# Kernel tuning notes

Measured on AMD Instinct MI355X. Metric: run time of the kernel, lower is better.

## Reference

```python
import jax, jax.numpy as jnp
import numpy as np

HIDDEN = 1024
ATT = 512

def _xavier(key, shape):
    fan_in, fan_out = shape[0], shape[1]
    bound = float(np.sqrt(6.0 / (fan_in + fan_out)))
    return jax.random.uniform(key, shape, jnp.float32, -bound, bound)

def setup_inputs() -> dict:
    key = jax.random.key(0)
    ks = jax.random.split(key, 7)
    B, P = 256, 196
    spatial_image = jax.random.normal(ks[0], (B, P, HIDDEN), jnp.float32)
    decoder_out = jax.random.normal(ks[1], (B, HIDDEN), jnp.float32)
    st = jax.random.normal(ks[2], (B, HIDDEN), jnp.float32)
    # weights stored as (in_dim, out_dim); math identical to torch Linear(x @ W.T)
    W_cnn = _xavier(ks[3], (HIDDEN, ATT))
    W_dec = _xavier(ks[4], (HIDDEN, ATT))
    W_sen = _xavier(ks[5], (HIDDEN, ATT))
    W_att = _xavier(ks[6], (ATT, 1))
    return {"spatial_image": spatial_image, "decoder_out": decoder_out, "st": st,
            "W_cnn": W_cnn, "W_dec": W_dec, "W_sen": W_sen, "W_att": W_att}

def reference(spatial_image, decoder_out, st, W_cnn, W_dec, W_sen, W_att):
    # dropout in eval mode (identity)
    cnn_out = jnp.einsum('bph,ha->bpa', spatial_image, W_cnn)   # (B,P,A)
    dec_out = decoder_out @ W_dec                                # (B,A)
    addition = jnp.tanh(cnn_out + dec_out[:, None, :])           # (B,P,A)
    zt = jnp.einsum('bpa,a->bp', addition, W_att[:, 0])          # (B,P)
    alpha_t = jax.nn.softmax(zt, axis=1)                         # (B,P)
    ct = jnp.einsum('bph,bp->bh', spatial_image, alpha_t)        # (B,H)
    sen = jnp.tanh(dec_out + st @ W_sen)                         # (B,A)
    out = sen @ W_att                                            # (B,1)
    concat = jnp.concatenate([zt, out], axis=1)                  # (B,P+1)
    alpha_hat = jax.nn.softmax(concat, axis=1)
    beta_t = alpha_hat[:, -1:]                                   # (B,1)
    c_hat = beta_t * st + (1.0 - beta_t) * ct                    # (B,H)
    return (alpha_t, beta_t, c_hat)
```

## Files before the change

kernel.cpp:

```cpp
#include <hip/hip_runtime.h>
#include <hip/hip_bf16.h>

#define BATCH   256
#define NP      196
#define HIDDEN  1024
#define ATT     512
#define M_TOTAL (BATCH * NP)
#define BM 128
#define BN 128
#define BK 32
#define NB_TILES (ATT / BN)
#define MT_TILES (M_TOTAL / BM)

typedef __attribute__((ext_vector_type(8))) short bf16x8v;
typedef __attribute__((ext_vector_type(4))) float f32x4;

__device__ inline unsigned short f2bf(float x) {
    unsigned int u = __float_as_uint(x);
    u += 0x7fffu + ((u >> 16) & 1u);
    return (unsigned short)(u >> 16);
}

__device__ __forceinline__ unsigned int pk2bf(float lo, float hi) {
    unsigned int r;
    asm("v_cvt_pk_bf16_f32 %0, %1, %2" : "=v"(r) : "v"(lo), "v"(hi));
    return r;
}

__device__ inline float fast_tanh(float x) {
    float e = __expf(2.0f * x);
    return 1.0f - 2.0f / (e + 1.0f);
}

__device__ __forceinline__ void glds16(const void* gsrc, void* ldst) {
    __builtin_amdgcn_global_load_lds(
        (const __attribute__((address_space(1))) unsigned int*)gsrc,
        (__attribute__((address_space(3))) unsigned int*)ldst,
        16, 0, 0);
}

__global__ void k0_arrange(const float* __restrict__ Wc, unsigned short* __restrict__ Wt) {
    int g = blockIdx.x * 256 + threadIdx.x;
    int nb   = g >> 14;
    int kt   = (g >> 9) & 31;
    int col  = (g >> 2) & 127;
    int slot = g & 3;
    int c    = slot ^ ((col & 7) >> 1);
    int kb   = kt * 32 + c * 8;
    int colg = nb * 128 + col;
    unsigned short v[8];
#pragma unroll
    for (int j = 0; j < 8; ++j) v[j] = f2bf(Wc[(size_t)(kb + j) * ATT + colg]);
    uint4 pk;
    pk.x = (unsigned int)v[0] | ((unsigned int)v[1] << 16);
    pk.y = (unsigned int)v[2] | ((unsigned int)v[3] << 16);
    pk.z = (unsigned int)v[4] | ((unsigned int)v[5] << 16);
    pk.w = (unsigned int)v[6] | ((unsigned int)v[7] << 16);
    *(uint4*)(Wt + (size_t)g * 8) = pk;
}

__global__ void k1_small(const float* __restrict__ dec_in, const float* __restrict__ st,
                         const float* __restrict__ Wdec,  const float* __restrict__ Wsen,
                         float* __restrict__ dec_out, float* __restrict__ stw) {
    const float* X = blockIdx.z ? st   : dec_in;
    const float* W = blockIdx.z ? Wsen : Wdec;
    float*       O = blockIdx.z ? stw  : dec_out;
    int ci = threadIdx.x & 31;
    int c0 = blockIdx.x * 128 + ci * 4;
    int b  = blockIdx.y * 8 + (threadIdx.x >> 5);
    const float* x = X + (size_t)b * HIDDEN;
    float4 acc = {0.f, 0.f, 0.f, 0.f};
    for (int k = 0; k < HIDDEN; k += 4) {
#pragma unroll
        for (int kk = 0; kk < 4; ++kk) {
            float4 w = *(const float4*)(W + (size_t)(k + kk) * ATT + c0);
            float a = x[k + kk];
            acc.x += a * w.x; acc.y += a * w.y; acc.z += a * w.z; acc.w += a * w.w;
        }
    }
    *(float4*)(O + (size_t)b * ATT + c0) = acc;
}

__global__ void __launch_bounds__(256, 3)
k2_fused_gemm(const float* __restrict__ A, const unsigned short* __restrict__ Wt,
              const float* __restrict__ dec, const float* __restrict__ Watt,
              float* __restrict__ ztp) {
    __shared__ __align__(16) char Abuf[2][8192];
    __shared__ __align__(16) char Bbuf[2][8192];
    __shared__ float zred[256];

    const int tid = threadIdx.x;
    const int w  = tid >> 6;
    const int l  = tid & 63;
    const int lg = l >> 4, ll = l & 15;
    const int wr = w >> 1, wc = w & 1;

    const int bid = (int)blockIdx.x;
    const int swz = (bid & 7) * 196 + (bid >> 3);
    const int mt = swz >> 2, nb = swz & 3;
    const int r0 = mt * BM;
    const int c0 = nb * BN;

    f32x4 acc[4][4];
#pragma unroll
    for (int m = 0; m < 4; ++m)
#pragma unroll
        for (int n = 0; n < 4; ++n) acc[m][n] = (f32x4){0.f, 0.f, 0.f, 0.f};

    const float* asrc = A + (size_t)(r0 + (tid >> 3)) * HIDDEN + (tid & 7) * 4;
    const int aw_off = ((tid >> 3) * 64)
                     + (((((tid >> 1) & 3) ^ ((tid >> 4) & 3))) << 4)
                     + ((tid & 1) * 8);

    const char* bimg = (const char*)Wt + (size_t)nb * (32 * 8192) + tid * 16;

    float4 avA[4], avB[4];

#define ALOADN(t, av) do {                                                     \
    _Pragma("unroll")                                                          \
    for (int j = 0; j < 4; ++j)                                                \
        (av)[j] = *(const float4*)(asrc + (size_t)j * 32 * HIDDEN + (t) * 32); \
} while (0)

#define BGLDS(t, buf) do {                                                     \
    glds16(bimg + (size_t)(t) * 8192,        (buf) + tid * 16);                \
    glds16(bimg + (size_t)(t) * 8192 + 4096, (buf) + 4096 + tid * 16);         \
} while (0)

#define AWRITE(av, buf) do {                                                   \
    _Pragma("unroll")                                                          \
    for (int j = 0; j < 4; ++j) {                                              \
        uint2 u;                                                               \
        u.x = pk2bf((av)[j].x, (av)[j].y);                                     \
        u.y = pk2bf((av)[j].z, (av)[j].w);                                     \
        *(uint2*)((buf) + j * 2048 + aw_off) = u;                              \
    }                                                                          \
} while (0)

#define COMPUTE(Ab, Bb) do {                                                   \
    const int fx = (ll >> 1) & 3;                                              \
    bf16x8v af[4], bfr[4];                                                     \
    _Pragma("unroll")                                                          \
    for (int m = 0; m < 4; ++m)                                                \
        af[m] = *(const bf16x8v*)((Ab) + (wr * 64 + m * 16 + ll) * 64 +        \
                                  ((lg ^ fx) << 4));                           \
    _Pragma("unroll")                                                          \
    for (int n = 0; n < 4; ++n)                                                \
        bfr[n] = *(const bf16x8v*)((Bb) + (wc * 64 + n * 16 + ll) * 64 +       \
                                   ((lg ^ fx) << 4));                          \
    _Pragma("unroll")                                                          \
    for (int m = 0; m < 4; ++m)                                                \
        _Pragma("unroll")                                                      \
        for (int n = 0; n < 4; ++n)                                            \
            acc[m][n] = __builtin_amdgcn_mfma_f32_16x16x32_bf16(               \
                af[m], bfr[n], acc[m][n], 0, 0, 0);                            \
} while (0)

#define WAITC asm volatile("s_waitcnt vmcnt(4) lgkmcnt(0)" ::: "memory")
#define BAR   __builtin_amdgcn_s_barrier()

    BGLDS(0, Bbuf[0]);
    ALOADN(0, avA);
    ALOADN(1, avB);
    AWRITE(avA, Abuf[0]);
    WAITC;
    BAR;

    for (int tp = 0; tp < 15; ++tp) {
        const int t = tp * 2;
        BGLDS(t + 1, Bbuf[1]);
        ALOADN(t + 2, avA);
        COMPUTE(Abuf[0], Bbuf[0]);
        AWRITE(avB, Abuf[1]);
        WAITC; BAR;
        BGLDS(t + 2, Bbuf[0]);
        ALOADN((t + 3 > 31 ? 31 : t + 3), avB);
        COMPUTE(Abuf[1], Bbuf[1]);
        AWRITE(avA, Abuf[0]);
        WAITC; BAR;
    }
    BGLDS(31, Bbuf[1]);
    COMPUTE(Abuf[0], Bbuf[0]);
    AWRITE(avB, Abuf[1]);
    asm volatile("s_waitcnt vmcnt(0) lgkmcnt(0)" ::: "memory");
    BAR;
    COMPUTE(Abuf[1], Bbuf[1]);

#undef ALOADN
#undef BGLDS
#undef AWRITE
#undef COMPUTE
#undef WAITC
#undef BAR

    const int clocal = wc * 64 + ll;
    float watt[4];
#pragma unroll
    for (int n = 0; n < 4; ++n) watt[n] = Watt[c0 + clocal + n * 16];

#pragma unroll
    for (int m = 0; m < 4; ++m) {
#pragma unroll
        for (int j = 0; j < 4; ++j) {
            int rl = wr * 64 + m * 16 + lg * 4 + j;
            int rowg = r0 + rl;
            int b = rowg / NP;
            const float* db = dec + (size_t)b * ATT + c0;
            float s = 0.f;
#pragma unroll
            for (int n = 0; n < 4; ++n)
                s += fast_tanh(acc[m][n][j] + db[clocal + n * 16]) * watt[n];
            s += __shfl_xor(s, 1);
            s += __shfl_xor(s, 2);
            s += __shfl_xor(s, 4);
            s += __shfl_xor(s, 8);
            if (ll == 0) zred[rl * 2 + wc] = s;
        }
    }
    __syncthreads();
    if (tid < 128) {
        float t = zred[tid * 2] + zred[tid * 2 + 1];
        ztp[(size_t)nb * M_TOTAL + r0 + tid] = t;
    }
}

__global__ void k3_softmax(const float* __restrict__ dec, const float* __restrict__ stw,
                           const float* __restrict__ Watt, const float* __restrict__ ztp,
                           float* __restrict__ out, float* __restrict__ beta_ws) {
    int b = blockIdx.x;
    int t = threadIdx.x;
    __shared__ float red[256];

    float p = 0.f;
#pragma unroll
    for (int c = t; c < ATT; c += 256)
        p += fast_tanh(dec[(size_t)b * ATT + c] + stw[(size_t)b * ATT + c]) * Watt[c];
    red[t] = p;
    __syncthreads();
    for (int s = 128; s > 0; s >>= 1) { if (t < s) red[t] += red[t + s]; __syncthreads(); }
    float outv = red[0];
    __syncthreads();

    float z = -1e30f;
    if (t < NP) {
        z = ztp[b * NP + t] + ztp[M_TOTAL + b * NP + t]
          + ztp[2 * M_TOTAL + b * NP + t] + ztp[3 * M_TOTAL + b * NP + t];
    }
    red[t] = z;
    __syncthreads();
    for (int s = 128; s > 0; s >>= 1) { if (t < s) red[t] = fmaxf(red[t], red[t + s]); __syncthreads(); }
    float m1 = red[0];
    __syncthreads();

    float e = (t < NP) ? __expf(z - m1) : 0.f;
    red[t] = e;
    __syncthreads();
    for (int s = 128; s > 0; s >>= 1) { if (t < s) red[t] += red[t + s]; __syncthreads(); }
    float s1 = red[0];

    if (t < NP) out[b * NP + t] = e / s1;

    if (t == 0) {
        float m2 = fmaxf(m1, outv);
        float s2 = s1 * __expf(m1 - m2) + __expf(outv - m2);
        float beta = __expf(outv - m2) / s2;
        out[M_TOTAL + b] = beta;
        beta_ws[b] = beta;
    }
}

__global__ void k4_ct(const float* __restrict__ spatial, const float* __restrict__ alpha,
                      float* __restrict__ ctp) {
    int q = blockIdx.x;
    int b = blockIdx.y;
    int t = threadIdx.x;
    __shared__ float al[49];
    if (t < 49) al[t] = alpha[b * NP + q * 49 + t];
    __syncthreads();
    const float* sp = spatial + (size_t)b * NP * HIDDEN + (size_t)q * 49 * HIDDEN + t * 4;
    float4 acc = {0.f, 0.f, 0.f, 0.f};
#pragma unroll 7
    for (int p = 0; p < 49; ++p) {
        float4 v = *(const float4*)(sp + (size_t)p * HIDDEN);
        float a = al[p];
        acc.x += a * v.x; acc.y += a * v.y; acc.z += a * v.z; acc.w += a * v.w;
    }
    *(float4*)(ctp + ((size_t)q * BATCH + b) * HIDDEN + t * 4) = acc;
}

__global__ void k5_chat(const float* __restrict__ st, const float* __restrict__ ctp,
                        const float* __restrict__ beta, float* __restrict__ chat) {
    int g = blockIdx.x * 256 + threadIdx.x;
    int b = g >> 8;
    int h0 = (g & 255) * 4;
    float be = beta[b];
    float4 s = *(const float4*)(st + (size_t)b * HIDDEN + h0);
    float4 c = {0.f, 0.f, 0.f, 0.f};
#pragma unroll
    for (int q = 0; q < 4; ++q) {
        float4 v = *(const float4*)(ctp + ((size_t)q * BATCH + b) * HIDDEN + h0);
        c.x += v.x; c.y += v.y; c.z += v.z; c.w += v.w;
    }
    float4 o;
    o.x = be * s.x + (1.f - be) * c.x;
    o.y = be * s.y + (1.f - be) * c.y;
    o.z = be * s.z + (1.f - be) * c.z;
    o.w = be * s.w + (1.f - be) * c.w;
    *(float4*)(chat + (size_t)b * HIDDEN + h0) = o;
}

extern "C" void kernel_launch(void* const* d_in, const int* in_sizes, int n_in,
                              void* d_out, int out_size, void* d_ws, size_t ws_size,
                              hipStream_t stream) {
    const float* spatial = (const float*)d_in[0];
    const float* decoder = (const float*)d_in[1];
    const float* st      = (const float*)d_in[2];
    const float* Wcnn    = (const float*)d_in[3];
    const float* Wdec    = (const float*)d_in[4];
    const float* Wsen    = (const float*)d_in[5];
    const float* Watt    = (const float*)d_in[6];
    float* out = (float*)d_out;

    char* ws = (char*)d_ws;
    unsigned short* Wt = (unsigned short*)(ws + 0);
    float* ztp  = (float*)(ws + 1048576);
    float* dec  = (float*)(ws + 1851392);
    float* stw  = (float*)(ws + 2375680);
    float* beta = (float*)(ws + 2899968);
    float* ctp  = (float*)(ws + 2901504);

    k0_arrange<<<256, 256, 0, stream>>>(Wcnn, Wt);
    k1_small<<<dim3(4, 32, 2), 256, 0, stream>>>(decoder, st, Wdec, Wsen, dec, stw);
    k2_fused_gemm<<<MT_TILES * NB_TILES, 256, 0, stream>>>(spatial, Wt, dec, Watt, ztp);
    k3_softmax<<<256, 256, 0, stream>>>(dec, stw, Watt, ztp, out, beta);
    k4_ct<<<dim3(4, 256), 256, 0, stream>>>(spatial, out, ctp);
    k5_chat<<<256, 256, 0, stream>>>(st, ctp, beta, out + M_TOTAL + BATCH);
}
```

Measured before the change: 199.0 us.

## Pre-convert spatial activations to swizzled bf16 tiles before the GEMM

Adds a pre-pass kernel that converts the fp32 spatial input into bf16 tiles in the same swizzled layout the GEMM uses in LDS. The GEMM then loads both operands straight into LDS with direct global-to-LDS copies, replacing the in-register conversion path. The new GEMM uses a single LDS buffer with two barriers per k-step instead of double buffering. This costs an extra full read and write pass over the activations and loses load/compute overlap, in exchange for halving A bytes inside the GEMM. The new path runs only when the workspace is large enough; otherwise the old kernel is used.

```diff
diff --git a/kernel.cpp b/kernel.cpp
--- a/kernel.cpp
+++ b/kernel.cpp
@@ -8,7 +8,6 @@
 #define M_TOTAL (BATCH * NP)
 #define BM 128
 #define BN 128
-#define BK 32
 #define NB_TILES (ATT / BN)
 #define MT_TILES (M_TOTAL / BM)
 
@@ -57,6 +56,26 @@
     pk.z = (unsigned int)v[4] | ((unsigned int)v[5] << 16);
     pk.w = (unsigned int)v[6] | ((unsigned int)v[7] << 16);
     *(uint4*)(Wt + (size_t)g * 8) = pk;
+}
+
+__global__ void k_pre(const float* __restrict__ sp, unsigned short* __restrict__ Ab) {
+    int g = blockIdx.x * 256 + threadIdx.x;
+    int mt   = g >> 14;
+    int r14  = g & 16383;
+    int kt   = r14 >> 9;
+    int r9   = r14 & 511;
+    int row  = r9 >> 2;
+    int slog = r9 & 3;
+    const float* src = sp + (size_t)(mt * 128 + row) * HIDDEN + kt * 32 + slog * 8;
+    float4 a = *(const float4*)(src);
+    float4 b = *(const float4*)(src + 4);
+    uint4 u;
+    u.x = pk2bf(a.x, a.y);
+    u.y = pk2bf(a.z, a.w);
+    u.z = pk2bf(b.x, b.y);
+    u.w = pk2bf(b.z, b.w);
+    int sphys = slog ^ ((row & 7) >> 1);
+    *(uint4*)((char*)Ab + (size_t)mt * 262144 + kt * 8192 + row * 64 + sphys * 16) = u;
 }
 
 __global__ void k1_small(const float* __restrict__ dec_in, const float* __restrict__ st,
@@ -82,11 +101,11 @@
 }
 
 __global__ void __launch_bounds__(256, 3)
-k2_fused_gemm(const float* __restrict__ A, const unsigned short* __restrict__ Wt,
-              const float* __restrict__ dec, const float* __restrict__ Watt,
-              float* __restrict__ ztp) {
-    __shared__ __align__(16) char Abuf[2][8192];
-    __shared__ __align__(16) char Bbuf[2][8192];
+k2_gemm(const unsigned short* __restrict__ Ab, const unsigned short* __restrict__ Wt,
+        const float* __restrict__ dec, const float* __restrict__ Watt,
+        float* __restrict__ ztp) {
+    __shared__ __align__(16) char As[8192];
+    __shared__ __align__(16) char Bs[8192];
     __shared__ float zred[256];
 
     const int tid = threadIdx.x;
@@ -107,11 +126,93 @@
 #pragma unroll
         for (int n = 0; n < 4; ++n) acc[m][n] = (f32x4){0.f, 0.f, 0.f, 0.f};
 
+    const char* aimg = (const char*)Ab + (size_t)mt * 262144;
+    const char* bimg = (const char*)Wt + (size_t)nb * 262144;
+    const int fx = (ll >> 1) & 3;
+
+    for (int kt = 0; kt < 32; ++kt) {
+        __syncthreads();
+        glds16(aimg + kt * 8192 +        tid * 16, As +        tid * 16);
+        glds16(aimg + kt * 8192 + 4096 + tid * 16, As + 4096 + tid * 16);
+        glds16(bimg + kt * 8192 +        tid * 16, Bs +        tid * 16);
+        glds16(bimg + kt * 8192 + 4096 + tid * 16, Bs + 4096 + tid * 16);
+        __syncthreads();
+
+        bf16x8v af[4], bfr[4];
+#pragma unroll
+        for (int m = 0; m < 4; ++m)
+            af[m] = *(const bf16x8v*)(As + (wr * 64 + m * 16 + ll) * 64 + ((lg ^ fx) << 4));
+#pragma unroll
+        for (int n = 0; n < 4; ++n)
+            bfr[n] = *(const bf16x8v*)(Bs + (wc * 64 + n * 16 + ll) * 64 + ((lg ^ fx) << 4));
+#pragma unroll
+        for (int m = 0; m < 4; ++m)
+#pragma unroll
+            for (int n = 0; n < 4; ++n)
+                acc[m][n] = __builtin_amdgcn_mfma_f32_16x16x32_bf16(af[m], bfr[n], acc[m][n], 0, 0, 0);
+    }
+
+    const int clocal = wc * 64 + ll;
+    float watt[4];
+#pragma unroll
+    for (int n = 0; n < 4; ++n) watt[n] = Watt[c0 + clocal + n * 16];
+
+#pragma unroll
+    for (int m = 0; m < 4; ++m) {
+#pragma unroll
+        for (int j = 0; j < 4; ++j) {
+            int rl = wr * 64 + m * 16 + lg * 4 + j;
+            int rowg = r0 + rl;
+            int b = rowg / NP;
+            const float* db = dec + (size_t)b * ATT + c0;
+            float s = 0.f;
+#pragma unroll
+            for (int n = 0; n < 4; ++n)
+                s += fast_tanh(acc[m][n][j] + db[clocal + n * 16]) * watt[n];
+            s += __shfl_xor(s, 1);
+            s += __shfl_xor(s, 2);
+            s += __shfl_xor(s, 4);
+            s += __shfl_xor(s, 8);
+            if (ll == 0) zred[rl * 2 + wc] = s;
+        }
+    }
+    __syncthreads();
+    if (tid < 128) {
+        float t = zred[tid * 2] + zred[tid * 2 + 1];
+        ztp[(size_t)nb * M_TOTAL + r0 + tid] = t;
+    }
+}
+
+__global__ void __launch_bounds__(256, 3)
+k2_fallback(const float* __restrict__ A, const unsigned short* __restrict__ Wt,
+            const float* __restrict__ dec, const float* __restrict__ Watt,
+            float* __restrict__ ztp) {
+    __shared__ __align__(16) char Abuf[2][8192];
+    __shared__ __align__(16) char Bbuf[2][8192];
+    __shared__ float zred[256];
+
+    const int tid = threadIdx.x;
+    const int w  = tid >> 6;
+    const int l  = tid & 63;
+    const int lg = l >> 4, ll = l & 15;
+    const int wr = w >> 1, wc = w & 1;
+
+    const int bid = (int)blockIdx.x;
+    const int swz = (bid & 7) * 196 + (bid >> 3);
+    const int mt = swz >> 2, nb = swz & 3;
+    const int r0 = mt * BM;
+    const int c0 = nb * BN;
+
+    f32x4 acc[4][4];
+#pragma unroll
+    for (int m = 0; m < 4; ++m)
+#pragma unroll
+        for (int n = 0; n < 4; ++n) acc[m][n] = (f32x4){0.f, 0.f, 0.f, 0.f};
+
     const float* asrc = A + (size_t)(r0 + (tid >> 3)) * HIDDEN + (tid & 7) * 4;
     const int aw_off = ((tid >> 3) * 64)
                      + (((((tid >> 1) & 3) ^ ((tid >> 4) & 3))) << 4)
                      + ((tid & 1) * 8);
-
     const char* bimg = (const char*)Wt + (size_t)nb * (32 * 8192) + tid * 16;
 
     float4 avA[4], avB[4];
@@ -121,12 +222,10 @@
     for (int j = 0; j < 4; ++j)                                                \
         (av)[j] = *(const float4*)(asrc + (size_t)j * 32 * HIDDEN + (t) * 32); \
 } while (0)
-
 #define BGLDS(t, buf) do {                                                     \
     glds16(bimg + (size_t)(t) * 8192,        (buf) + tid * 16);                \
     glds16(bimg + (size_t)(t) * 8192 + 4096, (buf) + 4096 + tid * 16);         \
 } while (0)
-
 #define AWRITE(av, buf) do {                                                   \
     _Pragma("unroll")                                                          \
     for (int j = 0; j < 4; ++j) {                                              \
@@ -136,7 +235,6 @@
         *(uint2*)((buf) + j * 2048 + aw_off) = u;                              \
     }                                                                          \
 } while (0)
-
 #define COMPUTE(Ab, Bb) do {                                                   \
     const int fx = (ll >> 1) & 3;                                              \
     bf16x8v af[4], bfr[4];                                                     \
@@ -155,7 +253,6 @@
             acc[m][n] = __builtin_amdgcn_mfma_f32_16x16x32_bf16(               \
                 af[m], bfr[n], acc[m][n], 0, 0, 0);                            \
 } while (0)
-
 #define WAITC asm volatile("s_waitcnt vmcnt(4) lgkmcnt(0)" ::: "memory")
 #define BAR   __builtin_amdgcn_s_barrier()
 
@@ -321,17 +418,28 @@
     const float* Watt    = (const float*)d_in[6];
     float* out = (float*)d_out;
 
+    const size_t AB_BYTES   = (size_t)MT_TILES * 32 * 8192;
+    const size_t SMALL_NEED = 1048576 + 802816 + 524288 + 524288 + 1024 + 4194304;
+    const int use_pre = (ws_size >= AB_BYTES + SMALL_NEED);
+
     char* ws = (char*)d_ws;
-    unsigned short* Wt = (unsigned short*)(ws + 0);
-    float* ztp  = (float*)(ws + 1048576);
-    float* dec  = (float*)(ws + 1851392);
-    float* stw  = (float*)(ws + 2375680);
-    float* beta = (float*)(ws + 2899968);
-    float* ctp  = (float*)(ws + 2901504);
+    size_t off = use_pre ? AB_BYTES : 0;
+    unsigned short* Ab = (unsigned short*)ws;
+    unsigned short* Wt = (unsigned short*)(ws + off); off += 1048576;
+    float* ztp  = (float*)(ws + off); off += 802816;
+    float* dec  = (float*)(ws + off); off += 524288;
+    float* stw  = (float*)(ws + off); off += 524288;
+    float* beta = (float*)(ws + off); off += 1024;
+    float* ctp  = (float*)(ws + off);
 
     k0_arrange<<<256, 256, 0, stream>>>(Wcnn, Wt);
     k1_small<<<dim3(4, 32, 2), 256, 0, stream>>>(decoder, st, Wdec, Wsen, dec, stw);
-    k2_fused_gemm<<<MT_TILES * NB_TILES, 256, 0, stream>>>(spatial, Wt, dec, Watt, ztp);
+    if (use_pre) {
+        k_pre<<<25088, 256, 0, stream>>>(spatial, Ab);
+        k2_gemm<<<MT_TILES * NB_TILES, 256, 0, stream>>>(Ab, Wt, dec, Watt, ztp);
+    } else {
+        k2_fallback<<<MT_TILES * NB_TILES, 256, 0, stream>>>(spatial, Wt, dec, Watt, ztp);
+    }
     k3_softmax<<<256, 256, 0, stream>>>(dec, stw, Watt, ztp, out, beta);
     k4_ct<<<dim3(4, 256), 256, 0, stream>>>(spatial, out, ctp);
     k5_chat<<<256, 256, 0, stream>>>(st, ctp, beta, out + M_TOTAL + BATCH);
```

After: 250.9 us. 26.1% more time.
